# Kernel tuning notes

Measured on AMD Instinct MI355X. Metric: run time of the kernel, lower is better.

Reference implementation:

```python
import jax, jax.numpy as jnp
import numpy as np

B, T, D, H, C = 256, 256, 512, 1024, 1000

def _xavier(key, shape):
    fan_in, fan_out = shape
    std = np.sqrt(2.0 / (fan_in + fan_out))
    return jax.random.normal(key, shape, dtype=jnp.float32) * std

def setup_inputs() -> dict:
    key = jax.random.key(0)
    ks = jax.random.split(key, 9)
    return {
        "x": jax.random.normal(ks[0], (B, T, D), dtype=jnp.float32),
        "W_z": _xavier(ks[1], (D, H)),
        "W_r": _xavier(ks[2], (D, H)),
        "W": _xavier(ks[3], (D, H)),
        "U_z": _xavier(ks[4], (H, H)),
        "U_r": _xavier(ks[5], (H, H)),
        "U": _xavier(ks[6], (H, H)),
        "W_ph": _xavier(ks[7], (H, C)),
        "b_p": jnp.zeros((C,), dtype=jnp.float32),
    }

def reference(x, W_z, W_r, W, U_z, U_r, U, W_ph, b_p):
    # Precompute input projections for all timesteps in 3 big GEMMs: [B,T,H]
    xz = jnp.einsum("btd,dh->bth", x, W_z)
    xr = jnp.einsum("btd,dh->bth", x, W_r)
    xh = jnp.einsum("btd,dh->bth", x, W)

    h0 = jnp.zeros((x.shape[0], U.shape[0]), dtype=x.dtype)

    def step(h, inp):
        xz_t, xr_t, xh_t = inp
        z = jax.nn.sigmoid(xz_t + h @ U_z)
        r = jax.nn.sigmoid(xr_t + h @ U_r)
        # NOTE: original applies reset gate AFTER the matmul: (h @ U) * r
        h_hat = jnp.tanh(xh_t + (h @ U) * r)
        h_new = z * h + (1.0 - z) * h_hat
        return h_new, None

    # scan over time: inputs shaped [T,B,H]
    h_last, _ = jax.lax.scan(
        step, h0,
        (xz.transpose(1, 0, 2), xr.transpose(1, 0, 2), xh.transpose(1, 0, 2)))

    p = h_last @ W_ph + b_p
    return jax.nn.log_softmax(p, axis=1)
```

## Files before the change

kernel.cpp:

```cpp
#include <hip/hip_runtime.h>
#include <hip/hip_bf16.h>

#define Bb 256
#define Tt 256
#define Dd 512
#define Hh 1024
#define Cc 1000

typedef short  bf16x8 __attribute__((ext_vector_type(8)));
typedef float  f32x4  __attribute__((ext_vector_type(4)));
typedef unsigned short u16x8 __attribute__((ext_vector_type(8)));
typedef unsigned long long u64;

#define NCI 144

#define REG_OFF  0
#define G0_OFF   64
#define LARR_OFF 128
#define AXC_OFF  4224
#define RDY_OFF  4352
#define ARR_OFF  4480
#define BAR_BYTES 32768
#define POLL_CAP 20000000

__device__ __forceinline__ unsigned short f2bf(float f) {
  unsigned u = __float_as_uint(f);
  u += 0x7FFFu + ((u >> 16) & 1u);
  return (unsigned short)(u >> 16);
}

__device__ __forceinline__ unsigned rmw_read(unsigned* p) {
  return __hip_atomic_fetch_add(p, 0u, __ATOMIC_RELAXED, __HIP_MEMORY_SCOPE_AGENT);
}
__device__ __forceinline__ void rmw_set(unsigned* p, unsigned v) {
  __hip_atomic_exchange(p, v, __ATOMIC_RELAXED, __HIP_MEMORY_SCOPE_AGENT);
}
__device__ __forceinline__ void rel_set(unsigned* p, unsigned v) {
  __hip_atomic_exchange(p, v, __ATOMIC_RELEASE, __HIP_MEMORY_SCOPE_AGENT);
}

__global__ void pack_weights(const float* __restrict__ Wz, const float* __restrict__ Wr,
                             const float* __restrict__ W,  const float* __restrict__ Uz,
                             const float* __restrict__ Ur, const float* __restrict__ U,
                             unsigned short* __restrict__ packed) {
  int tid = blockIdx.x * 256 + threadIdx.x;
  if (tid >= 64 * NCI * 64) return;
  int lane = tid & 63;
  int rest = tid >> 6;
  int ci   = rest % NCI;
  int c    = rest / NCI;
  int j    = (c << 4) + (lane & 15);
  int kg   = lane >> 4;
  const float* src; int kb;
  if      (ci < 16)  { src = Wz; kb = ci*32; }
  else if (ci < 48)  { src = Uz; kb = (ci-16)*32; }
  else if (ci < 64)  { src = Wr; kb = (ci-48)*32; }
  else if (ci < 96)  { src = Ur; kb = (ci-64)*32; }
  else if (ci < 112) { src = W;  kb = (ci-96)*32; }
  else               { src = U;  kb = (ci-112)*32; }
  int k0 = kb + kg*8;
  u16x8 o;
  #pragma unroll
  for (int e = 0; e < 8; ++e) o[e] = f2bf(src[(size_t)(k0+e)*Hh + j]);
  *(u16x8*)(packed + (size_t)tid*8) = o;
}

__global__ void cvt_x(const float* __restrict__ x, unsigned short* __restrict__ xb) {
  const int n4 = (Bb*Tt*Dd)/4;
  for (int i = blockIdx.x*256 + threadIdx.x; i < n4; i += gridDim.x*256) {
    f32x4 v = *(const f32x4*)(x + (size_t)i*4);
    unsigned short o[4];
    #pragma unroll
    for (int e = 0; e < 4; ++e) o[e] = f2bf(v[e]);
    *(u64*)(xb + (size_t)i*4) = *(u64*)o;
  }
}

template<bool XBF>
__global__ void __launch_bounds__(256, 1)
gru_scan(const float* __restrict__ x, const unsigned short* __restrict__ xb,
         const unsigned short* __restrict__ packed,
         float* __restrict__ hf, unsigned short* __restrict__ hb,
         unsigned* __restrict__ bar) {
  __shared__ short lds[NCI * 512];
  __shared__ int sh_idx, sh_xcc, sh_members;

  const int wg   = blockIdx.x;
  const int cblk = wg & 63;
  const int rblk = wg >> 6;
  const int tid  = threadIdx.x;
  const int lane = tid & 63;
  const int wave = tid >> 6;

  {
    const u16x8* s8 = (const u16x8*)(packed + (size_t)cblk * (NCI * 512));
    u16x8* d8 = (u16x8*)lds;
    #pragma unroll
    for (int i = 0; i < 36; ++i) d8[tid + i*256] = s8[tid + i*256];
  }

  unsigned xccr;
  asm("s_getreg_b32 %0, hwreg(20, 0, 4)" : "=s"(xccr));
  if (tid == 0) {
    int myx = (int)(xccr & 7u);
    unsigned idx = __hip_atomic_fetch_add(&bar[REG_OFF + myx*8], 1u,
                        __ATOMIC_RELAXED, __HIP_MEMORY_SCOPE_AGENT);
    sh_idx = (int)idx; sh_xcc = myx;
    __hip_atomic_fetch_add(&bar[G0_OFF], 1u, __ATOMIC_RELAXED, __HIP_MEMORY_SCOPE_AGENT);
  }
  __syncthreads();
  const int idx = sh_idx, myx = sh_xcc;
  if (tid == 0) {
    int cap = 0;
    while (rmw_read(&bar[G0_OFF]) < 256u && ++cap < POLL_CAP)
      __builtin_amdgcn_s_sleep(2);
    sh_members = (int)rmw_read(&bar[REG_OFF + myx*8]);
  }
  __syncthreads();
  const int  members  = sh_members;
  const bool fastmode = (members >= 1 && members <= 60);
  const bool leader   = (idx == 0);
  unsigned lanecnt = 0;
  if (wave == 0 && lane < 8) lanecnt = rmw_read(&bar[REG_OFF + lane*8]);

  const int arow = lane & 15;
  const int kg   = lane >> 4;
  const int b    = rblk*64 + wave*16 + arow;
  const int crow = rblk*64 + wave*16 + kg*4;
  const int j    = (cblk << 4) + arow;

  const float*          xrow  = x  + (size_t)b * Tt * Dd;
  const unsigned short* xbrow = xb + (size_t)b * Tt * Dd;

  f32x4 hold = {0.f,0.f,0.f,0.f};

  bf16x8 xa[16];
  if constexpr (XBF) {
    #pragma unroll
    for (int kk = 0; kk < 16; ++kk) xa[kk] = *(const bf16x8*)(xbrow + kk*32 + kg*8);
  } else {
    #pragma unroll
    for (int kk = 0; kk < 16; ++kk) {
      f32x4 v0 = *(const f32x4*)(xrow + kk*32 + kg*8);
      f32x4 v1 = *(const f32x4*)(xrow + kk*32 + kg*8 + 4);
      bf16x8 a;
      #pragma unroll
      for (int e = 0; e < 4; ++e) { ((unsigned short*)&a)[e] = f2bf(v0[e]); ((unsigned short*)&a)[e+4] = f2bf(v1[e]); }
      xa[kk] = a;
    }
  }

  for (int t = 0; t < Tt; ++t) {
    if (t > 0 && wave == 0) {
      const unsigned tgt = (unsigned)t;
      if (fastmode) {
        if (leader) {
          int cap = 0;
          for (;;) {
            unsigned v = (lane < members)
                ? rmw_read(&bar[LARR_OFF + (myx*64 + lane)*8]) : tgt;
            if (__all((int)(v >= tgt))) break;
            if (++cap > POLL_CAP) break;
            __builtin_amdgcn_s_sleep(1);
          }
          if (lane == 0) rel_set(&bar[AXC_OFF + myx*8], tgt);
          cap = 0;
          for (;;) {
            unsigned v = (lane < 8 && lanecnt > 0)
                ? rmw_read(&bar[AXC_OFF + lane*8]) : tgt;
            if (__all((int)(v >= tgt))) break;
            if (++cap > POLL_CAP) break;
            __builtin_amdgcn_s_sleep(1);
          }
          __builtin_amdgcn_fence(__ATOMIC_ACQUIRE, "agent");
          if (lane == 0) rmw_set(&bar[RDY_OFF + myx*8], tgt);
        } else {
          int cap = 0;
          while (rmw_read(&bar[RDY_OFF + myx*8]) < tgt && ++cap < POLL_CAP)
            __builtin_amdgcn_s_sleep(1);
        }
      } else {
        int cap = 0;
        for (;;) {
          unsigned v = rmw_read(&bar[ARR_OFF + (rblk*64 + lane)*8]);
          if (__all((int)(v >= tgt))) break;
          if (++cap > POLL_CAP) break;
          __builtin_amdgcn_s_sleep(1);
        }
        __builtin_amdgcn_fence(__ATOMIC_ACQUIRE, "agent");
      }
    }

    f32x4 az  = {0.f,0.f,0.f,0.f};
    f32x4 arr = {0.f,0.f,0.f,0.f};
    f32x4 axh = {0.f,0.f,0.f,0.f};
    f32x4 ahu = {0.f,0.f,0.f,0.f};

    #pragma unroll
    for (int kk = 0; kk < 16; ++kk) {
      bf16x8 bz = *(const bf16x8*)&lds[(0  + kk)*512 + lane*8];
      bf16x8 br = *(const bf16x8*)&lds[(48 + kk)*512 + lane*8];
      bf16x8 bx = *(const bf16x8*)&lds[(96 + kk)*512 + lane*8];
      az  = __builtin_amdgcn_mfma_f32_16x16x32_bf16(xa[kk], bz, az , 0,0,0);
      arr = __builtin_amdgcn_mfma_f32_16x16x32_bf16(xa[kk], br, arr, 0,0,0);
      axh = __builtin_amdgcn_mfma_f32_16x16x32_bf16(xa[kk], bx, axh, 0,0,0);
    }

    if (t + 1 < Tt) {
      if constexpr (XBF) {
        const unsigned short* xt = xbrow + (size_t)(t+1)*Dd;
        #pragma unroll
        for (int kk = 0; kk < 16; ++kk) xa[kk] = *(const bf16x8*)(xt + kk*32 + kg*8);
      } else {
        const float* xt = xrow + (size_t)(t+1)*Dd;
        #pragma unroll
        for (int kk = 0; kk < 16; ++kk) {
          f32x4 v0 = *(const f32x4*)(xt + kk*32 + kg*8);
          f32x4 v1 = *(const f32x4*)(xt + kk*32 + kg*8 + 4);
          bf16x8 a;
          #pragma unroll
          for (int e = 0; e < 4; ++e) { ((unsigned short*)&a)[e] = f2bf(v0[e]); ((unsigned short*)&a)[e+4] = f2bf(v1[e]); }
          xa[kk] = a;
        }
      }
    }

    if (t > 0) {
      __syncthreads();

      const unsigned short* hrow = hb + (size_t)(t & 1)*(Bb*Hh) + (size_t)b*Hh;
      bf16x8 ha[32];
      #pragma unroll
      for (int kk = 0; kk < 32; ++kk)
        ha[kk] = *(const bf16x8*)(hrow + kk*32 + kg*8);

      #pragma unroll
      for (int kk = 0; kk < 32; ++kk) {
        bf16x8 bz = *(const bf16x8*)&lds[(16  + kk)*512 + lane*8];
        bf16x8 br = *(const bf16x8*)&lds[(64  + kk)*512 + lane*8];
        bf16x8 bu = *(const bf16x8*)&lds[(112 + kk)*512 + lane*8];
        az  = __builtin_amdgcn_mfma_f32_16x16x32_bf16(ha[kk], bz, az , 0,0,0);
        arr = __builtin_amdgcn_mfma_f32_16x16x32_bf16(ha[kk], br, arr, 0,0,0);
        ahu = __builtin_amdgcn_mfma_f32_16x16x32_bf16(ha[kk], bu, ahu, 0,0,0);
      }
    }

    unsigned short hv[4];
    #pragma unroll
    for (int e = 0; e < 4; ++e) {
      float z  = 1.f / (1.f + __expf(-az[e]));
      float r  = 1.f / (1.f + __expf(-arr[e]));
      float u  = axh[e] + ahu[e] * r;
      float hh = 2.f / (1.f + __expf(-2.f * u)) - 1.f;
      float hn = z*hold[e] + (1.f - z)*hh;
      hold[e]  = hn;
      hv[e]    = f2bf(hn);
    }

    if (t < Tt - 1) {
      unsigned short* hbw = hb + (size_t)((t+1) & 1)*(Bb*Hh);
      #pragma unroll
      for (int e = 0; e < 4; ++e) hbw[(size_t)(crow+e)*Hh + j] = hv[e];
      __syncthreads();
      if (tid == 0) {
        unsigned tv = (unsigned)(t + 1);
        rmw_set(&bar[LARR_OFF + (myx*64 + idx)*8], tv);
        if (!fastmode) rel_set(&bar[ARR_OFF + wg*8], tv);
      }
    } else {
      #pragma unroll
      for (int e = 0; e < 4; ++e) hf[(size_t)(crow+e)*Hh + j] = hold[e];
    }
  }
}

__global__ void classifier(const float* __restrict__ h, const float* __restrict__ Wph,
                           const float* __restrict__ bp, float* __restrict__ out) {
  __shared__ float hsm[8 * Hh];
  const int cb = blockIdx.x, bbk = blockIdx.y;
  const int tid = threadIdx.x;
  const float* h0 = h + (size_t)bbk * 8 * Hh;
  for (int i = tid; i < 8 * Hh; i += 256) {
    int r = i >> 10, k = i & (Hh - 1);
    hsm[k*8 + r] = h0[i];
  }
  __syncthreads();
  int c = cb*256 + tid;
  bool act = c < Cc;
  float acc[8] = {0,0,0,0,0,0,0,0};
  for (int k = 0; k < Hh; ++k) {
    float w = act ? Wph[(size_t)k*Cc + c] : 0.f;
    f32x4 h0v = *(const f32x4*)&hsm[k*8];
    f32x4 h1v = *(const f32x4*)&hsm[k*8 + 4];
    acc[0] += h0v[0]*w; acc[1] += h0v[1]*w; acc[2] += h0v[2]*w; acc[3] += h0v[3]*w;
    acc[4] += h1v[0]*w; acc[5] += h1v[1]*w; acc[6] += h1v[2]*w; acc[7] += h1v[3]*w;
  }
  if (act) {
    float bias = bp[c];
    #pragma unroll
    for (int r = 0; r < 8; ++r) out[(size_t)(bbk*8 + r)*Cc + c] = acc[r] + bias;
  }
}

__global__ void logsoftmax(float* __restrict__ out) {
  __shared__ float sm[4];
  float* row = out + (size_t)blockIdx.x * Cc;
  const int tid = threadIdx.x;
  float m = -3.4e38f;
  for (int i = tid; i < Cc; i += 256) m = fmaxf(m, row[i]);
  #pragma unroll
  for (int o = 32; o; o >>= 1) m = fmaxf(m, __shfl_down(m, o, 64));
  if ((tid & 63) == 0) sm[tid >> 6] = m;
  __syncthreads();
  m = fmaxf(fmaxf(sm[0], sm[1]), fmaxf(sm[2], sm[3]));
  __syncthreads();
  float s = 0.f;
  for (int i = tid; i < Cc; i += 256) s += __expf(row[i] - m);
  #pragma unroll
  for (int o = 32; o; o >>= 1) s += __shfl_down(s, o, 64);
  if ((tid & 63) == 0) sm[tid >> 6] = s;
  __syncthreads();
  s = sm[0] + sm[1] + sm[2] + sm[3];
  float lse = m + __logf(s);
  for (int i = tid; i < Cc; i += 256) row[i] -= lse;
}

extern "C" void kernel_launch(void* const* d_in, const int* in_sizes, int n_in,
                              void* d_out, int out_size, void* d_ws, size_t ws_size,
                              hipStream_t stream) {
  (void)in_sizes; (void)n_in; (void)out_size;
  const float* x   = (const float*)d_in[0];
  const float* Wz  = (const float*)d_in[1];
  const float* Wr  = (const float*)d_in[2];
  const float* W   = (const float*)d_in[3];
  const float* Uz  = (const float*)d_in[4];
  const float* Ur  = (const float*)d_in[5];
  const float* U   = (const float*)d_in[6];
  const float* Wph = (const float*)d_in[7];
  const float* bp  = (const float*)d_in[8];
  float* out = (float*)d_out;

  char* ws = (char*)d_ws;
  const size_t OFF_PACK = 0;
  const size_t OFF_HF   = 9437184;
  const size_t OFF_HB   = OFF_HF + 1048576;
  const size_t OFF_BAR  = OFF_HB + 1048576;
  const size_t OFF_XB   = OFF_BAR + 32768;
  unsigned short* packed = (unsigned short*)(ws + OFF_PACK);
  float*          hf     = (float*)(ws + OFF_HF);
  unsigned short* hb     = (unsigned short*)(ws + OFF_HB);
  unsigned*       bar    = (unsigned*)(ws + OFF_BAR);
  unsigned short* xbm    = (unsigned short*)(ws + OFF_XB);
  const bool xbf = ws_size >= OFF_XB + (size_t)67108864;

  hipMemsetAsync(bar, 0, BAR_BYTES, stream);
  pack_weights<<<dim3(2304), dim3(256), 0, stream>>>(Wz, Wr, W, Uz, Ur, U, packed);
  if (xbf) cvt_x<<<dim3(2048), dim3(256), 0, stream>>>(x, xbm);

  void* args[] = { (void*)&x, (void*)&xbm, (void*)&packed, (void*)&hf, (void*)&hb, (void*)&bar };
  if (xbf) {
    hipLaunchCooperativeKernel(reinterpret_cast<void*>(&gru_scan<true>),
                               dim3(256), dim3(256), args, 0, stream);
  } else {
    hipLaunchCooperativeKernel(reinterpret_cast<void*>(&gru_scan<false>),
                               dim3(256), dim3(256), args, 0, stream);
  }

  classifier<<<dim3(4, 32), dim3(256), 0, stream>>>(hf, Wph, bp, out);
  logsoftmax<<<dim3(256), dim3(256), 0, stream>>>(out);
}
```

Measured before the change: 3.008 ms.

## Map batch row groups to XCD pairs to shrink per-step barrier scope

When every XCD has exactly 32 workgroups, each batch row group (64 rows) is assigned to a pair of XCDs. Each workgroup's column block is derived from its XCD parity and index within that XCD, so the per-timestep barrier only waits on the partner XCD instead of all eight. The fallback slow per-workgroup arrival path is removed and replaced by the hierarchical leader scheme for all cases. This is meant to cut cross-XCD synchronization latency in the 256-step recurrence. The risk is correctness if the workgroup distribution is uneven, because the fallback then relies on the all-XCD path with members counts above 60.

```diff
diff --git a/kernel.cpp b/kernel.cpp
--- a/kernel.cpp
+++ b/kernel.cpp
@@ -19,7 +19,6 @@
 #define LARR_OFF 128
 #define AXC_OFF  4224
 #define RDY_OFF  4352
-#define ARR_OFF  4480
 #define BAR_BYTES 32768
 #define POLL_CAP 20000000
 
@@ -83,21 +82,12 @@
          float* __restrict__ hf, unsigned short* __restrict__ hb,
          unsigned* __restrict__ bar) {
   __shared__ short lds[NCI * 512];
-  __shared__ int sh_idx, sh_xcc, sh_members;
+  __shared__ int sh_idx, sh_xcc, sh_members, sh_ok;
 
   const int wg   = blockIdx.x;
-  const int cblk = wg & 63;
-  const int rblk = wg >> 6;
   const int tid  = threadIdx.x;
   const int lane = tid & 63;
   const int wave = tid >> 6;
-
-  {
-    const u16x8* s8 = (const u16x8*)(packed + (size_t)cblk * (NCI * 512));
-    u16x8* d8 = (u16x8*)lds;
-    #pragma unroll
-    for (int i = 0; i < 36; ++i) d8[tid + i*256] = s8[tid + i*256];
-  }
 
   unsigned xccr;
   asm("s_getreg_b32 %0, hwreg(20, 0, 4)" : "=s"(xccr));
@@ -114,19 +104,38 @@
     int cap = 0;
     while (rmw_read(&bar[G0_OFF]) < 256u && ++cap < POLL_CAP)
       __builtin_amdgcn_s_sleep(2);
-    sh_members = (int)rmw_read(&bar[REG_OFF + myx*8]);
-  }
-  __syncthreads();
+    int pairok = 1;
+    unsigned cm = 0;
+    for (int i = 0; i < 8; ++i) {
+      unsigned c = rmw_read(&bar[REG_OFF + i*8]);
+      if (c != 32u) pairok = 0;
+      if (i == myx) cm = c;
+    }
+    sh_ok = pairok;
+    sh_members = (int)cm;
+  }
+  __syncthreads();
+  const bool pairmode = (sh_ok != 0);
   const int  members  = sh_members;
-  const bool fastmode = (members >= 1 && members <= 60);
   const bool leader   = (idx == 0);
   unsigned lanecnt = 0;
   if (wave == 0 && lane < 8) lanecnt = rmw_read(&bar[REG_OFF + lane*8]);
 
+  const int rgroup = pairmode ? (myx >> 1) : (wg >> 6);
+  const int cblk   = pairmode ? ((myx & 1) * 32 + idx) : (wg & 63);
+
+  {
+    const u16x8* s8 = (const u16x8*)(packed + (size_t)cblk * (NCI * 512));
+    u16x8* d8 = (u16x8*)lds;
+    #pragma unroll
+    for (int i = 0; i < 36; ++i) d8[tid + i*256] = s8[tid + i*256];
+  }
+  __syncthreads();
+
   const int arow = lane & 15;
   const int kg   = lane >> 4;
-  const int b    = rblk*64 + wave*16 + arow;
-  const int crow = rblk*64 + wave*16 + kg*4;
+  const int b    = rgroup*64 + wave*16 + arow;
+  const int crow = rgroup*64 + wave*16 + kg*4;
   const int j    = (cblk << 4) + arow;
 
   const float*          xrow  = x  + (size_t)b * Tt * Dd;
@@ -153,18 +162,26 @@
   for (int t = 0; t < Tt; ++t) {
     if (t > 0 && wave == 0) {
       const unsigned tgt = (unsigned)t;
-      if (fastmode) {
-        if (leader) {
-          int cap = 0;
+      if (leader) {
+        int cap = 0;
+        for (;;) {
+          unsigned v = (lane < members)
+              ? rmw_read(&bar[LARR_OFF + (myx*64 + lane)*8]) : tgt;
+          if (__all((int)(v >= tgt))) break;
+          if (++cap > POLL_CAP) break;
+          __builtin_amdgcn_s_sleep(1);
+        }
+        if (lane == 0) rel_set(&bar[AXC_OFF + myx*8], tgt);
+        cap = 0;
+        if (pairmode) {
           for (;;) {
-            unsigned v = (lane < members)
-                ? rmw_read(&bar[LARR_OFF + (myx*64 + lane)*8]) : tgt;
+            unsigned v = (lane == 0)
+                ? rmw_read(&bar[AXC_OFF + (myx^1)*8]) : tgt;
             if (__all((int)(v >= tgt))) break;
             if (++cap > POLL_CAP) break;
             __builtin_amdgcn_s_sleep(1);
           }
-          if (lane == 0) rel_set(&bar[AXC_OFF + myx*8], tgt);
-          cap = 0;
+        } else {
           for (;;) {
             unsigned v = (lane < 8 && lanecnt > 0)
                 ? rmw_read(&bar[AXC_OFF + lane*8]) : tgt;
@@ -172,22 +189,13 @@
             if (++cap > POLL_CAP) break;
             __builtin_amdgcn_s_sleep(1);
           }
-          __builtin_amdgcn_fence(__ATOMIC_ACQUIRE, "agent");
-          if (lane == 0) rmw_set(&bar[RDY_OFF + myx*8], tgt);
-        } else {
-          int cap = 0;
-          while (rmw_read(&bar[RDY_OFF + myx*8]) < tgt && ++cap < POLL_CAP)
-            __builtin_amdgcn_s_sleep(1);
         }
+        __builtin_amdgcn_fence(__ATOMIC_ACQUIRE, "agent");
+        if (lane == 0) rmw_set(&bar[RDY_OFF + myx*8], tgt);
       } else {
         int cap = 0;
-        for (;;) {
-          unsigned v = rmw_read(&bar[ARR_OFF + (rblk*64 + lane)*8]);
-          if (__all((int)(v >= tgt))) break;
-          if (++cap > POLL_CAP) break;
+        while (rmw_read(&bar[RDY_OFF + myx*8]) < tgt && ++cap < POLL_CAP)
           __builtin_amdgcn_s_sleep(1);
-        }
-        __builtin_amdgcn_fence(__ATOMIC_ACQUIRE, "agent");
       }
     }
 
@@ -262,11 +270,8 @@
       #pragma unroll
       for (int e = 0; e < 4; ++e) hbw[(size_t)(crow+e)*Hh + j] = hv[e];
       __syncthreads();
-      if (tid == 0) {
-        unsigned tv = (unsigned)(t + 1);
-        rmw_set(&bar[LARR_OFF + (myx*64 + idx)*8], tv);
-        if (!fastmode) rel_set(&bar[ARR_OFF + wg*8], tv);
-      }
+      if (tid == 0)
+        rmw_set(&bar[LARR_OFF + (myx*64 + idx)*8], (unsigned)(t + 1));
     } else {
       #pragma unroll
       for (int e = 0; e < 4; ++e) hf[(size_t)(crow+e)*Hh + j] = hold[e];
```

After: 2.511 ms, median of 2. -16.5%, faster.
